# Kernel optimization log

Measured on AMD Instinct MI355X. Metric: run time of the kernel, lower is better.

## Reference

```python
import jax, jax.numpy as jnp
import numpy as np
from jax import lax

K = 16               # kNN neighbors
SAMPLING_RATIO = 0.25
BN_EPS = 1e-5


def farthest_point_sample(p, M):
    """Iterative FPS. p: (B,N,3) -> (B,M) int32 indices. Starts at index 0 (as pointnet2_ops)."""
    B, N, _ = p.shape
    batch = jnp.arange(B)

    def step(carry, _):
        dist, last = carry                       # dist: (B,N) min sq-dist to selected set
        sel = p[batch, last]                     # (B,3) last selected point
        d = jnp.sum((p - sel[:, None, :]) ** 2, axis=-1)  # (B,N)
        dist = jnp.minimum(dist, d)
        nxt = jnp.argmax(dist, axis=-1).astype(jnp.int32)
        return (dist, nxt), nxt

    first = jnp.zeros((B,), jnp.int32)
    init_dist = jnp.full((B, N), 1e10, jnp.float32)
    (_, _), rest = lax.scan(step, (init_dist, first), None, length=M - 1)  # rest: (M-1,B)
    return jnp.concatenate([first[None, :], rest], axis=0).T  # (B,M)


def knn(p2, p1, k):
    """For each query in p2:(B,M,3) find k nearest in p1:(B,N,3). Returns (B,M,k) indices."""
    # squared distances via ||a||^2 + ||b||^2 - 2 a.b  -> (B,M,N)
    d = (jnp.sum(p2 * p2, -1)[:, :, None]
         + jnp.sum(p1 * p1, -1)[:, None, :]
         - 2.0 * jnp.einsum('bmd,bnd->bmn', p2, p1))
    _, idx = lax.top_k(-d, k)
    return idx


def setup_inputs() -> dict:
    key = jax.random.key(0)
    k1, k2, k3 = jax.random.split(key, 3)
    B, N, Cin, Cout = 8, 8192, 64, 128
    x = jax.random.normal(k1, (B, N, Cin), jnp.float32)
    p1 = jax.random.normal(k2, (B, N, 3), jnp.float32)
    W = jax.random.normal(k3, (Cout, Cin), jnp.float32) * 0.1  # Conv1d k=1, no bias
    gamma = jnp.ones((Cout,), jnp.float32)   # BatchNorm weight
    beta = jnp.zeros((Cout,), jnp.float32)   # BatchNorm bias
    return {"x": x, "p1": p1, "W": W, "gamma": gamma, "beta": beta}


def reference(x, p1, W, gamma, beta):
    B, N, Cin = x.shape
    M = int(N * SAMPLING_RATIO)

    fps_idx = farthest_point_sample(p1, M)                         # (B,M)
    p2 = jnp.take_along_axis(p1, fps_idx[:, :, None], axis=1)      # (B,M,3)
    neighbors = knn(p2, p1, K)                                     # (B,M,K)

    # pointwise conv (1x1) + BatchNorm1d (train-mode batch stats over B*N) + ReLU
    h = jnp.einsum('bnc,oc->bno', x, W)                            # (B,N,Cout)
    mean = jnp.mean(h, axis=(0, 1))
    var = jnp.var(h, axis=(0, 1))
    h = gamma * (h - mean) * lax.rsqrt(var + BN_EPS) + beta
    h = jax.nn.relu(h)

    Cout = h.shape[-1]
    feats = jnp.take_along_axis(h, neighbors.reshape(B, M * K, 1), axis=1)
    feats = feats.reshape(B, M, K, Cout)                           # index_points gather
    y = jnp.max(feats, axis=2)                                     # max-pool over k neighbors
    return y, p2
```

## Files before the change

### kernel.cpp

```cpp
#include <hip/hip_runtime.h>
#include <cstdint>

#define B_   8
#define N_   8192
#define M_   2048
#define CIN  64
#define COUT 128

typedef unsigned long long u64;

__device__ __forceinline__ float sq3(float dx, float dy, float dz) {
    return __fadd_rn(__fadd_rn(__fmul_rn(dx, dx), __fmul_rn(dy, dy)), __fmul_rn(dz, dz));
}

__global__ __launch_bounds__(256) void phase1_kernel(const float* __restrict__ p1, float* __restrict__ p2,
                                                     const float* __restrict__ x, const float* __restrict__ W,
                                                     float* __restrict__ h) {
    __shared__ __align__(16) char smem[98368];
    int t = threadIdx.x;

    if (blockIdx.x < B_) {
        float2* lds_xy = (float2*)smem;
        float*  lds_z  = (float*)(smem + 65536);
        double* wbest  = (double*)(smem + 98304);

        int b = blockIdx.x;
        const float* pb = p1 + (size_t)b * N_ * 3;
        float* p2b = p2 + (size_t)b * M_ * 3;
        int lane = t & 63, wave = t >> 6;

        for (int i = t; i < N_; i += 256) {
            lds_xy[i] = make_float2(pb[3 * i], pb[3 * i + 1]);
            lds_z[i]  = pb[3 * i + 2];
        }
        __syncthreads();

        float px[32], py[32], pz[32], dist[32];
#pragma unroll
        for (int j = 0; j < 32; ++j) {
            int idx = t + j * 256;
            float2 xy = lds_xy[idx];
            px[j] = xy.x; py[j] = xy.y; pz[j] = lds_z[idx];
            dist[j] = 1e10f;
        }

        float2 s0 = lds_xy[0];
        float sx = s0.x, sy = s0.y, sz = lds_z[0];
        if (t == 0) { p2b[0] = sx; p2b[1] = sy; p2b[2] = sz; }

        for (int i = 1; i < M_; ++i) {
            float bestv = -1.0f; int besti = 0;
#pragma unroll
            for (int j = 0; j < 32; ++j) {
                float d = sq3(__fsub_rn(px[j], sx), __fsub_rn(py[j], sy), __fsub_rn(pz[j], sz));
                float nd = fminf(dist[j], d);
                dist[j] = nd;
                if (nd > bestv) { bestv = nd; besti = t + j * 256; }
            }
            double key = __longlong_as_double(__double_as_longlong((double)bestv) | (u64)(8191 - besti));
#pragma unroll
            for (int off = 32; off >= 1; off >>= 1)
                key = fmax(key, __shfl_xor(key, off));
            int buf = (i & 1) << 2;
            if (lane == 0) wbest[buf + wave] = key;
            __syncthreads();
            double2 a = *(double2*)&wbest[buf];
            double2 c = *(double2*)&wbest[buf + 2];
            double km = fmax(fmax(a.x, a.y), fmax(c.x, c.y));
            int w = 8191 - (int)(__double_as_longlong(km) & 0x1fff);
            float2 sxy = lds_xy[w];
            sx = sxy.x; sy = sxy.y; sz = lds_z[w];
            if (t == 0) { p2b[3 * i] = sx; p2b[3 * i + 1] = sy; p2b[3 * i + 2] = sz; }
        }
    } else {
        float (*xs)[65] = (float (*)[65])smem;
        float (*ws)[65] = (float (*)[65])(smem + 16640);
        size_t rowBase = (size_t)(blockIdx.x - B_) * 64;
        for (int idx = t; idx < COUT * CIN; idx += 256) ws[idx >> 6][idx & 63] = W[idx];
        const float* xb = x + rowBase * CIN;
        for (int idx = t; idx < 64 * CIN; idx += 256) xs[idx >> 6][idx & 63] = xb[idx];
        __syncthreads();
        int r0 = (t & 15) * 4, c0 = (t >> 4) * 8;
        float acc[4][8];
#pragma unroll
        for (int i = 0; i < 4; ++i)
#pragma unroll
            for (int j = 0; j < 8; ++j) acc[i][j] = 0.f;
        for (int k = 0; k < CIN; ++k) {
            float xv[4], wvv[8];
#pragma unroll
            for (int i = 0; i < 4; ++i) xv[i] = xs[r0 + i][k];
#pragma unroll
            for (int j = 0; j < 8; ++j) wvv[j] = ws[c0 + j][k];
#pragma unroll
            for (int i = 0; i < 4; ++i)
#pragma unroll
                for (int j = 0; j < 8; ++j) acc[i][j] = fmaf(xv[i], wvv[j], acc[i][j]);
        }
#pragma unroll
        for (int i = 0; i < 4; ++i) {
            size_t o = (rowBase + r0 + i) * COUT + c0;
            *(float4*)&h[o]     = make_float4(acc[i][0], acc[i][1], acc[i][2], acc[i][3]);
            *(float4*)&h[o + 4] = make_float4(acc[i][4], acc[i][5], acc[i][6], acc[i][7]);
        }
    }
}

__global__ __launch_bounds__(256) void bn_partial(const float* __restrict__ h, float* __restrict__ psum,
                                                  float* __restrict__ psq) {
    int t = threadIdx.x;
    int c = t & 127, half = t >> 7;
    size_t base = (size_t)blockIdx.x * 256;
    float s = 0.f, q = 0.f;
    for (int it = 0; it < 128; ++it) {
        float v = h[(base + it * 2 + half) * COUT + c];
        s += v; q = fmaf(v, v, q);
    }
    __shared__ float ls[256], lq[256];
    ls[t] = s; lq[t] = q;
    __syncthreads();
    if (t < 128) {
        psum[blockIdx.x * 128 + c] = ls[t] + ls[t + 128];
        psq[blockIdx.x * 128 + c]  = lq[t] + lq[t + 128];
    }
}

__global__ void bn_final(const float* __restrict__ psum, const float* __restrict__ psq,
                         const float* __restrict__ gamma, const float* __restrict__ beta,
                         float* __restrict__ bns) {
    int c = threadIdx.x;
    float s = 0.f, q = 0.f;
    for (int i = 0; i < 256; ++i) { s += psum[i * 128 + c]; q += psq[i * 128 + c]; }
    float mean = s / 65536.0f;
    float var  = q / 65536.0f - mean * mean;
    float sc = gamma[c] * rsqrtf(var + 1e-5f);
    bns[c] = sc;
    bns[128 + c] = beta[c] - mean * sc;
}

__global__ __launch_bounds__(256) void knn_kernel(const float* __restrict__ p1, const float* __restrict__ p2,
                                                  const float* __restrict__ h, const float* __restrict__ bns,
                                                  float* __restrict__ y) {
    int q = blockIdx.x * 4 + (threadIdx.x >> 6);
    int lane = threadIdx.x & 63;
    int b = q >> 11;
    const float* pb = p1 + (size_t)b * N_ * 3;
    const float* pq = p2 + (size_t)q * 3;
    float qx = pq[0], qy = pq[1], qz = pq[2];
    float sqq = __fadd_rn(__fadd_rn(__fmul_rn(qx, qx), __fmul_rn(qy, qy)), __fmul_rn(qz, qz));

    float ld = 1e30f; int li = 0;
    float tau = 1e30f;

    for (int c0 = 0; c0 < N_; c0 += 64) {
        int cand = c0 + lane;
        float ax = pb[3 * cand], ay = pb[3 * cand + 1], az = pb[3 * cand + 2];
        float s1 = __fadd_rn(__fadd_rn(__fmul_rn(ax, ax), __fmul_rn(ay, ay)), __fmul_rn(az, az));
        float dt = __fadd_rn(__fadd_rn(__fmul_rn(ax, qx), __fmul_rn(ay, qy)), __fmul_rn(az, qz));
        float d  = __fsub_rn(__fadd_rn(sqq, s1), __fmul_rn(2.0f, dt));
        unsigned long long mk = __ballot(d < tau);
        while (mk) {
            int l = __ffsll((unsigned long long)mk) - 1;
            mk &= mk - 1;
            float dd = __shfl(d, l);
            int   ii = c0 + l;
            int pos = __popcll(__ballot(ld <= dd) & 0xFFFFull);
            if (pos < 16) {
                float pd = __shfl_up(ld, 1);
                int   pi = __shfl_up(li, 1);
                if (lane < 16) {
                    if (lane > pos) { ld = pd; li = pi; }
                    if (lane == pos) { ld = dd; li = ii; }
                }
                tau = __shfl(ld, 15);
            }
        }
    }

    int c = lane << 1;
    float sc0 = bns[c], sc1 = bns[c + 1];
    float sh0 = bns[128 + c], sh1 = bns[128 + c + 1];
    float a0 = -1e30f, a1 = -1e30f;
#pragma unroll
    for (int t16 = 0; t16 < 16; ++t16) {
        int nb = __shfl(li, t16);
        const float* hp = h + (((size_t)(b * N_ + nb)) << 7) + c;
        float h0 = hp[0], h1 = hp[1];
        a0 = fmaxf(a0, fmaf(h0, sc0, sh0));
        a1 = fmaxf(a1, fmaf(h1, sc1, sh1));
    }
    float2 out = make_float2(fmaxf(a0, 0.f), fmaxf(a1, 0.f));
    *(float2*)&y[((size_t)q << 7) + c] = out;
}

extern "C" void kernel_launch(void* const* d_in, const int* in_sizes, int n_in,
                              void* d_out, int out_size, void* d_ws, size_t ws_size,
                              hipStream_t stream) {
    const float* x     = (const float*)d_in[0];
    const float* p1    = (const float*)d_in[1];
    const float* W     = (const float*)d_in[2];
    const float* gamma = (const float*)d_in[3];
    const float* beta  = (const float*)d_in[4];

    float* y  = (float*)d_out;
    float* p2 = y + (size_t)B_ * M_ * COUT;

    float* h    = (float*)d_ws;
    float* psum = h + (size_t)B_ * N_ * COUT;
    float* psq  = psum + 256 * 128;
    float* bns  = psq + 256 * 128;

    phase1_kernel<<<B_ + (B_ * N_) / 64, 256, 0, stream>>>(p1, p2, x, W, h);
    bn_partial<<<256, 256, 0, stream>>>(h, psum, psq);
    bn_final<<<1, 128, 0, stream>>>(psum, psq, gamma, beta, bns);
    knn_kernel<<<(B_ * M_) / 4, 256, 0, stream>>>(p1, p2, h, bns, y);
}
```

Before: 2.262 ms.

## Restructure FPS argmax into float max reduction plus atomicMin index resolution

Replaces the per-iteration packed double-key argmax (64-bit shuffles) in farthest point sampling with a float-only max computed through DPP row operations. A second pass lets only threads holding the global max scan their distances for the matching index and resolve ties with an LDS atomicMin. Output writes of selected points are rotated across waves and delayed by one iteration. This adds a second barrier per iteration and a rescan of 32 registers on the winning threads, in exchange for cheaper reductions.

```diff
diff --git a/kernel.cpp b/kernel.cpp
--- a/kernel.cpp
+++ b/kernel.cpp
@@ -7,22 +7,28 @@
 #define CIN  64
 #define COUT 128
 
-typedef unsigned long long u64;
-
 __device__ __forceinline__ float sq3(float dx, float dy, float dz) {
     return __fadd_rn(__fadd_rn(__fmul_rn(dx, dx), __fmul_rn(dy, dy)), __fmul_rn(dz, dz));
 }
 
-__global__ __launch_bounds__(256) void phase1_kernel(const float* __restrict__ p1, float* __restrict__ p2,
-                                                     const float* __restrict__ x, const float* __restrict__ W,
-                                                     float* __restrict__ h) {
+template<int CTRL>
+__device__ __forceinline__ float dppmaxf(float x) {
+    int b = __float_as_int(x);
+    int p = __builtin_amdgcn_update_dpp(b, b, CTRL, 0xf, 0xf, false);
+    return fmaxf(x, __int_as_float(p));
+}
+
+__global__ __launch_bounds__(256, 1) void phase1_kernel(const float* __restrict__ p1, float* __restrict__ p2,
+                                                        const float* __restrict__ x, const float* __restrict__ W,
+                                                        float* __restrict__ h) {
     __shared__ __align__(16) char smem[98368];
     int t = threadIdx.x;
 
     if (blockIdx.x < B_) {
         float2* lds_xy = (float2*)smem;
         float*  lds_z  = (float*)(smem + 65536);
-        double* wbest  = (double*)(smem + 98304);
+        float*  wmax   = (float*)(smem + 98304);
+        int*    slot   = (int*)(smem + 98304 + 32);
 
         int b = blockIdx.x;
         const float* pb = p1 + (size_t)b * N_ * 3;
@@ -33,6 +39,7 @@
             lds_xy[i] = make_float2(pb[3 * i], pb[3 * i + 1]);
             lds_z[i]  = pb[3 * i + 2];
         }
+        if (t < 2) slot[t] = 0x7fffffff;
         __syncthreads();
 
         float px[32], py[32], pz[32], dist[32];
@@ -46,31 +53,45 @@
 
         float2 s0 = lds_xy[0];
         float sx = s0.x, sy = s0.y, sz = lds_z[0];
-        if (t == 0) { p2b[0] = sx; p2b[1] = sy; p2b[2] = sz; }
 
         for (int i = 1; i < M_; ++i) {
-            float bestv = -1.0f; int besti = 0;
+            if (t == ((i & 3) << 6)) {
+                p2b[3 * (i - 1)] = sx; p2b[3 * (i - 1) + 1] = sy; p2b[3 * (i - 1) + 2] = sz;
+            }
+            int buf = i & 1;
+            float bestv = -1.0f;
 #pragma unroll
             for (int j = 0; j < 32; ++j) {
                 float d = sq3(__fsub_rn(px[j], sx), __fsub_rn(py[j], sy), __fsub_rn(pz[j], sz));
                 float nd = fminf(dist[j], d);
                 dist[j] = nd;
-                if (nd > bestv) { bestv = nd; besti = t + j * 256; }
-            }
-            double key = __longlong_as_double(__double_as_longlong((double)bestv) | (u64)(8191 - besti));
-#pragma unroll
-            for (int off = 32; off >= 1; off >>= 1)
-                key = fmax(key, __shfl_xor(key, off));
-            int buf = (i & 1) << 2;
-            if (lane == 0) wbest[buf + wave] = key;
+                bestv = fmaxf(bestv, nd);
+            }
+            bestv = dppmaxf<0x121>(bestv);
+            bestv = dppmaxf<0x122>(bestv);
+            bestv = dppmaxf<0x124>(bestv);
+            bestv = dppmaxf<0x128>(bestv);
+            bestv = dppmaxf<0x142>(bestv);
+            bestv = dppmaxf<0x143>(bestv);
+            if (lane == 63) wmax[buf * 4 + wave] = bestv;
             __syncthreads();
-            double2 a = *(double2*)&wbest[buf];
-            double2 c = *(double2*)&wbest[buf + 2];
-            double km = fmax(fmax(a.x, a.y), fmax(c.x, c.y));
-            int w = 8191 - (int)(__double_as_longlong(km) & 0x1fff);
+            float4 wm = *(float4*)&wmax[buf * 4];
+            float gmax = fmaxf(fmaxf(wm.x, wm.y), fmaxf(wm.z, wm.w));
+            if (bestv >= gmax) {
+                int myidx = 0x7fffffff;
+#pragma unroll
+                for (int j = 31; j >= 0; --j)
+                    if (dist[j] == gmax) myidx = t + j * 256;
+                atomicMin(&slot[buf], myidx);
+            }
+            __syncthreads();
+            int w = slot[buf];
+            if (t == 64) slot[buf ^ 1] = 0x7fffffff;
             float2 sxy = lds_xy[w];
             sx = sxy.x; sy = sxy.y; sz = lds_z[w];
-            if (t == 0) { p2b[3 * i] = sx; p2b[3 * i + 1] = sy; p2b[3 * i + 2] = sz; }
+        }
+        if (t == 0) {
+            p2b[3 * (M_ - 1)] = sx; p2b[3 * (M_ - 1) + 1] = sy; p2b[3 * (M_ - 1) + 2] = sz;
         }
     } else {
         float (*xs)[65] = (float (*)[65])smem;
```

Measured after the change: 4.589 ms. 2.03x slower.
